# Kernel optimization log

Measured on AMD Instinct MI355X. Metric: run time of the kernel, lower is better.

Reference implementation:

```python
import jax, jax.numpy as jnp
import numpy as np

C = 96          # channels
N_STATE = 16    # d_state
EXPAND = 2
DI = EXPAND * C # d_inner = 192
D_CONV = 4
DT_RANK = 6     # ceil(C / 16)
EPS = 1e-5


def setup_inputs() -> dict:
    key = jax.random.key(0)
    ks = jax.random.split(key, 9)
    rn = lambda k, sh, s: jax.random.normal(k, sh, jnp.float32) * s
    inp = {
        "x": rn(ks[0], (1, C, 32, 32, 32), 1.0),
        # per-direction params, stacked along axis 0 in order (z, y, x)
        "ln_g": jnp.ones((3, C), jnp.float32),
        "ln_b": jnp.zeros((3, C), jnp.float32),
        "Win": rn(ks[1], (3, C, 2 * DI), 0.05),          # in_proj (no bias)
        "Wconv": rn(ks[2], (3, DI, 1, D_CONV), 0.2),     # depthwise conv1d
        "bconv": rn(ks[3], (3, DI), 0.02),
        "Wxp": rn(ks[4], (3, DI, DT_RANK + 2 * N_STATE), 0.05),  # x_proj
        "Wdt": rn(ks[5], (3, DT_RANK, DI), 0.1),         # dt_proj
        "bdt": rn(ks[6], (3, DI), 0.02),
        "A_log": jnp.log(jnp.broadcast_to(
            jnp.arange(1, N_STATE + 1, dtype=jnp.float32), (3, DI, N_STATE))),
        "Dskip": jnp.ones((3, DI), jnp.float32),
        "Wout": rn(ks[7], (3, DI, C), 0.05),             # out_proj (no bias)
        "alpha": jnp.ones((3,), jnp.float32),
    }
    return inp


def _layernorm(x, g, b):
    m = jnp.mean(x, axis=-1, keepdims=True)
    v = jnp.mean(jnp.square(x - m), axis=-1, keepdims=True)
    return (x - m) * jax.lax.rsqrt(v + EPS) * g + b


def _selective_scan(u, delta, A, Bm, Cm, Dskip):
    # u, delta: (N, L, DI); A: (DI, n); Bm, Cm: (N, L, n); Dskip: (DI,)
    def step(s, inp):
        d_t, B_t, C_t, u_t = inp                 # (N,DI),(N,n),(N,n),(N,DI)
        dA = jnp.exp(d_t[..., None] * A)         # (N, DI, n)
        dBu = d_t[..., None] * B_t[:, None, :] * u_t[..., None]
        s = dA * s + dBu                         # (N, DI, n)
        y = jnp.einsum('pdn,pn->pd', s, C_t)     # (N, DI)
        return s, y
    s0 = jnp.zeros((u.shape[0], A.shape[0], A.shape[1]), u.dtype)
    xs = (jnp.swapaxes(delta, 0, 1), jnp.swapaxes(Bm, 0, 1),
          jnp.swapaxes(Cm, 0, 1), jnp.swapaxes(u, 0, 1))
    _, ys = jax.lax.scan(step, s0, xs)           # ys: (L, N, DI)
    return jnp.swapaxes(ys, 0, 1) + u * Dskip


def _mamba_block(x, Win, Wconv, bconv, Wxp, Wdt, bdt, A_log, Dskip, Wout):
    # x: (N, L, C)
    xr = x @ Win                                  # (N, L, 2*DI)
    xm, res = jnp.split(xr, 2, axis=-1)
    # causal depthwise conv1d (torch pads d_conv-1 both sides then slices [:L])
    xc = jax.lax.conv_general_dilated(
        jnp.swapaxes(xm, 1, 2), Wconv, window_strides=(1,),
        padding=[(D_CONV - 1, 0)], feature_group_count=DI,
        dimension_numbers=('NCH', 'OIH', 'NCH')) + bconv[None, :, None]
    xm = jax.nn.silu(jnp.swapaxes(xc, 1, 2))      # (N, L, DI)
    x_dbl = xm @ Wxp
    dt = x_dbl[..., :DT_RANK]
    Bm = x_dbl[..., DT_RANK:DT_RANK + N_STATE]
    Cm = x_dbl[..., DT_RANK + N_STATE:]
    delta = jax.nn.softplus(dt @ Wdt + bdt)       # (N, L, DI)
    A = -jnp.exp(A_log)
    y = _selective_scan(xm, delta, A, Bm, Cm, Dskip)
    y = y * jax.nn.silu(res)
    return y @ Wout                               # (N, L, C)


def reference(x, ln_g, ln_b, Win, Wconv, bconv, Wxp, Wdt, bdt, A_log, Dskip, Wout, alpha):
    B, Cc, Dd, Hh, Ww = x.shape

    def run(i, xs):
        xs = _layernorm(xs, ln_g[i], ln_b[i])
        return _mamba_block(xs, Win[i], Wconv[i], bconv[i], Wxp[i], Wdt[i],
                            bdt[i], A_log[i], Dskip[i], Wout[i])

    # axial: scan depth D for each (h, w)
    xz = run(0, jnp.transpose(x, (0, 3, 4, 2, 1)).reshape(B * Hh * Ww, Dd, Cc))
    xz = jnp.transpose(xz.reshape(B, Hh, Ww, Dd, Cc), (0, 4, 3, 1, 2))
    # coronal: scan height H for each (d, w)
    xy = run(1, jnp.transpose(x, (0, 2, 4, 3, 1)).reshape(B * Dd * Ww, Hh, Cc))
    xy = jnp.transpose(xy.reshape(B, Dd, Ww, Hh, Cc), (0, 4, 1, 3, 2))
    # sagittal: scan width W for each (d, h)
    xx = run(2, jnp.transpose(x, (0, 2, 3, 4, 1)).reshape(B * Dd * Hh, Ww, Cc))
    xx = jnp.transpose(xx.reshape(B, Dd, Hh, Ww, Cc), (0, 4, 1, 2, 3))

    w = jax.nn.softmax(alpha)
    return w[0] * xz + w[1] * xy + w[2] * xx
```

## Files before the change

kernel.cpp:

```cpp
#include <hip/hip_runtime.h>
#include <hip/hip_bf16.h>


#define EPS_ 1e-5f

typedef __bf16 bf16x8 __attribute__((ext_vector_type(8)));
typedef float f32x4 __attribute__((ext_vector_type(4)));
typedef float f32x2 __attribute__((ext_vector_type(2)));
union U8b { uint4 u; bf16x8 v; };

__device__ __forceinline__ float silu_f(float v) { return v / (1.f + __expf(-v)); }
__device__ __forceinline__ bf16x8 ld_frag(const __hip_bfloat16* p) {
    U8b t; t.u = *(const uint4*)p; return t.v;
}

__global__ __launch_bounds__(256) void cvt_kernel(
    const float* __restrict__ Win, const float* __restrict__ Wxp,
    const float* __restrict__ Wout, __hip_bfloat16* __restrict__ ws)
{
    const int id = blockIdx.x * 256 + threadIdx.x;
    if (id < 110592) {
        const int d = id / 36864, r = id % 36864, n = r / 96, k = r % 96;
        ws[id] = __float2bfloat16(Win[d * 36864 + k * 384 + n]);
    } else if (id < 138240) {
        const int t = id - 110592;
        const int d = t / 9216, r = t % 9216, n = r / 192, k = r % 192;
        const float v = (n < 38) ? Wxp[d * 7296 + k * 38 + n] : 0.f;
        ws[id] = __float2bfloat16(v);
    } else {
        const int t = id - 138240;
        const int d = t / 18432, r = t % 18432, n = r / 192, k = r % 192;
        ws[id] = __float2bfloat16(Wout[d * 18432 + k * 96 + n]);
    }
}

template<bool PARTIAL>
__global__ __launch_bounds__(256, 4) void tdm_kernel(
    const float* __restrict__ x,     const float* __restrict__ ln_g,  const float* __restrict__ ln_b,
    const float* __restrict__ Wconv, const float* __restrict__ bconv,
    const float* __restrict__ Wdt,   const float* __restrict__ bdt,
    const float* __restrict__ Dskip,
    const float* __restrict__ alpha, const __hip_bfloat16* __restrict__ ws,
    float* __restrict__ pp,          float* __restrict__ out)
{
    __shared__ __align__(16) char sbuf[6656];
    __shared__ __align__(16) __hip_bfloat16 xu[32 * 200];
    __shared__ __align__(16) __hip_bfloat16 gyb[32 * 200];
    __hip_bfloat16* const aT    = (__hip_bfloat16*)sbuf;
    float*          const xdbuf = (float*)sbuf;

    const int tid = threadIdx.x;
    const int bid = blockIdx.x;
    const int wid = (bid & 7) * 384 + (bid >> 3);
    const int dir = wid >> 10;
    const int s   = wid & 1023;

    const float* gi = ln_g  + dir * 96;
    const float* bi = ln_b  + dir * 96;
    const float* Wc = Wconv + dir * 192 * 4;
    const float* bc = bconv + dir * 192;
    const float* Wd = Wdt   + dir * 6 * 192;
    const float* bd = bdt   + dir * 192;
    const float* Dk = Dskip + dir * 192;

    int base0, tmul;
    {
        const int hi = s >> 5, lo = s & 31;
        if (dir == 0)      { base0 = hi * 32 + lo;        tmul = 1024; }
        else if (dir == 1) { base0 = hi * 1024 + lo;      tmul = 32;   }
        else               { base0 = hi * 1024 + lo * 32; tmul = 1;    }
    }

    {
        const int row = tid >> 3;
        const int sub = tid & 7;
        float xv[12];
        float sum = 0.f, sq = 0.f;
        #pragma unroll
        for (int j = 0; j < 12; ++j) {
            const int c = sub * 12 + j;
            const float v = x[c * 32768 + row * tmul + base0];
            xv[j] = v; sum += v; sq += v * v;
        }
        #pragma unroll
        for (int m = 1; m < 8; m <<= 1) {
            sum += __shfl_xor(sum, m);
            sq  += __shfl_xor(sq, m);
        }
        const float mean = sum * (1.f / 96.f);
        const float var  = sq * (1.f / 96.f) - mean * mean;
        const float rstd = rsqrtf(var + EPS_);
        #pragma unroll
        for (int j = 0; j < 12; ++j) {
            const int c = sub * 12 + j;
            aT[row * 104 + c] = __float2bfloat16((xv[j] - mean) * rstd * gi[c] + bi[c]);
        }
    }
    __syncthreads();

    const int w  = tid >> 6;
    const int l  = tid & 63;
    const int lg = l >> 4;
    const int lm = l & 15;

    {
        const __hip_bfloat16* WT = ws + dir * 36864;
        #pragma unroll 1
        for (int mt = 0; mt < 2; ++mt) {
            bf16x8 aF[3];
            #pragma unroll
            for (int ks = 0; ks < 3; ++ks)
                aF[ks] = ld_frag(aT + (lm + 16 * mt) * 104 + 32 * ks + 8 * lg);
            f32x4 acc[6];
            #pragma unroll
            for (int nt = 0; nt < 6; ++nt) acc[nt] = (f32x4){0.f, 0.f, 0.f, 0.f};
            #pragma unroll
            for (int nt = 0; nt < 6; ++nt) {
                const int n = 96 * w + 16 * nt + lm;
                #pragma unroll
                for (int ks = 0; ks < 3; ++ks) {
                    const bf16x8 bF = ld_frag(WT + n * 96 + 32 * ks + 8 * lg);
                    acc[nt] = __builtin_amdgcn_mfma_f32_16x16x32_bf16(aF[ks], bF, acc[nt], 0, 0, 0);
                }
            }
            #pragma unroll
            for (int nt = 0; nt < 6; ++nt)
                #pragma unroll
                for (int reg = 0; reg < 4; ++reg) {
                    const int t   = 16 * mt + 4 * lg + reg;
                    const int col = 96 * w + 16 * nt + lm;
                    const float v = acc[nt][reg];
                    if (w < 2) xu[t * 200 + col] = __float2bfloat16(v);
                    else       gyb[t * 200 + (col - 192)] = __float2bfloat16(silu_f(v));
                }
        }
    }
    __syncthreads();

    if (tid < 192) {
        const int d = tid;
        const float4 wc = *(const float4*)&Wc[d * 4];
        const float bcd = bc[d];
        float w0 = 0.f, w1 = 0.f, w2 = 0.f;
        #pragma unroll
        for (int t = 0; t < 32; ++t) {
            const float xv = __bfloat162float(xu[t * 200 + d]);
            const float a  = bcd + w0 * wc.x + w1 * wc.y + w2 * wc.z + xv * wc.w;
            w0 = w1; w1 = w2; w2 = xv;
            xu[t * 200 + d] = __float2bfloat16(silu_f(a));
        }
    }
    __syncthreads();

    {
        const __hip_bfloat16* WT = ws + 110592 + dir * 9216;
        #pragma unroll
        for (int p = 0; p < 2; ++p) {
            const int T = (p == 0) ? w : (w < 2 ? w + 4 : -1);
            if (T >= 0) {
                const int mt = T / 3, nt = T % 3;
                f32x4 acc = (f32x4){0.f, 0.f, 0.f, 0.f};
                #pragma unroll
                for (int ks = 0; ks < 6; ++ks) {
                    const bf16x8 aF = ld_frag(xu + (lm + 16 * mt) * 200 + 32 * ks + 8 * lg);
                    const bf16x8 bF = ld_frag(WT + (16 * nt + lm) * 192 + 32 * ks + 8 * lg);
                    acc = __builtin_amdgcn_mfma_f32_16x16x32_bf16(aF, bF, acc, 0, 0, 0);
                }
                const int n = 16 * nt + lm;
                if (n < 38) {
                    const int col = (n < 6) ? n : n + 2;
                    #pragma unroll
                    for (int reg = 0; reg < 4; ++reg)
                        xdbuf[(16 * mt + 4 * lg + reg) * 40 + col] = acc[reg];
                }
            }
        }
    }
    __syncthreads();

    if (tid < 192) {
        const int d = tid;
        const f32x2 wd01 = {Wd[0 * 192 + d], Wd[1 * 192 + d]};
        const f32x2 wd23 = {Wd[2 * 192 + d], Wd[3 * 192 + d]};
        const f32x2 wd45 = {Wd[4 * 192 + d], Wd[5 * 192 + d]};
        const float bdd = bd[d], dsk = Dk[d];
        f32x2 st2[8];
        #pragma unroll
        for (int n = 0; n < 8; ++n) st2[n] = (f32x2){0.f, 0.f};
        for (int t = 0; t < 32; ++t) {
            const f32x4* row = (const f32x4*)(xdbuf + t * 40);
            const f32x4 q0 = row[0];
            const f32x4 q1 = row[1];
            f32x2 dt2 = (f32x2){q0.x, q0.y} * wd01;
            dt2 += (f32x2){q0.z, q0.w} * wd23;
            dt2 += (f32x2){q1.x, q1.y} * wd45;
            const float dt_ = bdd + dt2.x + dt2.y;
            const float p   = __expf(dt_);
            const float r   = __builtin_amdgcn_rcpf(1.f + p);
            const float dlt = (dt_ > 15.f) ? dt_ : __logf(1.f + p);
            const float ut  = __bfloat162float(xu[t * 200 + d]);
            const float du  = dlt * ut;
            const float r2s = r * r;
            const f32x2 r2v = {r2s, r2s};
            const f32x2 du2 = {du, du};
            f32x2 fp = {r, r2s};
            f32x2 y2 = {0.f, 0.f};
            #pragma unroll
            for (int g = 0; g < 4; ++g) {
                const f32x4 qB = row[2 + g];
                const f32x4 qC = row[6 + g];
                st2[2 * g]     = fp * st2[2 * g]     + du2 * (f32x2){qB.x, qB.y};
                y2            += st2[2 * g]     * (f32x2){qC.x, qC.y};
                fp            *= r2v;
                st2[2 * g + 1] = fp * st2[2 * g + 1] + du2 * (f32x2){qB.z, qB.w};
                y2            += st2[2 * g + 1] * (f32x2){qC.z, qC.w};
                fp            *= r2v;
            }
            const float y = y2.x + y2.y;
            const float gate = __bfloat162float(gyb[t * 200 + d]);
            gyb[t * 200 + d] = __float2bfloat16((y + ut * dsk) * gate);
        }
    }
    __syncthreads();

    {
        const __hip_bfloat16* WT = ws + 138240 + dir * 18432;
        const int mt = w >> 1, ntb = 3 * (w & 1);
        bf16x8 aF[6];
        #pragma unroll
        for (int ks = 0; ks < 6; ++ks)
            aF[ks] = ld_frag(gyb + (lm + 16 * mt) * 200 + 32 * ks + 8 * lg);
        const float e0 = __expf(alpha[0]), e1 = __expf(alpha[1]), e2 = __expf(alpha[2]);
        const float wgt = ((dir == 0) ? e0 : (dir == 1) ? e1 : e2) / (e0 + e1 + e2);
        #pragma unroll
        for (int nt3 = 0; nt3 < 3; ++nt3) {
            const int nt = ntb + nt3;
            f32x4 acc = (f32x4){0.f, 0.f, 0.f, 0.f};
            #pragma unroll
            for (int ks = 0; ks < 6; ++ks) {
                const bf16x8 bF = ld_frag(WT + (16 * nt + lm) * 192 + 32 * ks + 8 * lg);
                acc = __builtin_amdgcn_mfma_f32_16x16x32_bf16(aF[ks], bF, acc, 0, 0, 0);
            }
            const int j = 16 * nt + lm;
            if (PARTIAL) {
                if (dir < 2) {
                    float* dst = pp + (size_t)wid * 3072;
                    #pragma unroll
                    for (int reg = 0; reg < 4; ++reg) {
                        const int t = 16 * mt + 4 * lg + reg;
                        dst[t * 96 + j] = acc[reg] * wgt;
                    }
                } else {
                    #pragma unroll
                    for (int reg = 0; reg < 4; ++reg) {
                        const int t = 16 * mt + 4 * lg + reg;
                        out[j * 32768 + s * 32 + t] = acc[reg] * wgt;
                    }
                }
            } else {
                #pragma unroll
                for (int reg = 0; reg < 4; ++reg) {
                    const int t = 16 * mt + 4 * lg + reg;
                    atomicAdd(&out[j * 32768 + t * tmul + base0], acc[reg] * wgt);
                }
            }
        }
    }
}

__global__ __launch_bounds__(256) void red_kernel(const float* __restrict__ pp,
                                                  float* __restrict__ out)
{
    __shared__ float tile[96 * 33];
    const int d = blockIdx.x >> 5, h = blockIdx.x & 31;
    {
        const int w  = threadIdx.x >> 3;
        const int cs = (threadIdx.x & 7) * 12;
        const float* p0 = pp +           ((h * 32 + w) * 32 + d) * 96 + cs;
        const float* p1 = pp + 3145728 + ((d * 32 + w) * 32 + h) * 96 + cs;
        #pragma unroll
        for (int i = 0; i < 12; ++i)
            tile[(cs + i) * 33 + w] = p0[i] + p1[i];
    }
    __syncthreads();
    {
        const int w2 = threadIdx.x & 31;
        const int c0 = (threadIdx.x >> 5) * 12;
        #pragma unroll
        for (int i = 0; i < 12; ++i) {
            const int c = c0 + i;
            const int o = c * 32768 + d * 1024 + h * 32 + w2;
            out[o] = out[o] + tile[c * 33 + w2];
        }
    }
}

extern "C" void kernel_launch(void* const* d_in, const int* in_sizes, int n_in,
                              void* d_out, int out_size, void* d_ws, size_t ws_size,
                              hipStream_t stream) {
    (void)in_sizes; (void)n_in;
    __hip_bfloat16* ws = (__hip_bfloat16*)d_ws;
    float* pp = (float*)((char*)d_ws + 393216);
    const bool partial = (ws_size >= 25559040u);

    cvt_kernel<<<dim3(756), dim3(256), 0, stream>>>(
        (const float*)d_in[3], (const float*)d_in[6], (const float*)d_in[11], ws);

    if (partial) {
        tdm_kernel<true><<<dim3(3072), dim3(256), 0, stream>>>(
            (const float*)d_in[0],  (const float*)d_in[1],  (const float*)d_in[2],
            (const float*)d_in[4],  (const float*)d_in[5],
            (const float*)d_in[7],  (const float*)d_in[8],
            (const float*)d_in[10],
            (const float*)d_in[12], ws, pp, (float*)d_out);
        red_kernel<<<dim3(1024), dim3(256), 0, stream>>>(pp, (float*)d_out);
    } else {
        hipMemsetAsync(d_out, 0, (size_t)out_size * sizeof(float), stream);
        tdm_kernel<false><<<dim3(3072), dim3(256), 0, stream>>>(
            (const float*)d_in[0],  (const float*)d_in[1],  (const float*)d_in[2],
            (const float*)d_in[4],  (const float*)d_in[5],
            (const float*)d_in[7],  (const float*)d_in[8],
            (const float*)d_in[10],
            (const float*)d_in[12], ws, pp, (float*)d_out);
    }
}
```

Baseline: 205.8 us.

## Store partial direction outputs in bf16 and process three sequences per block

The partial-result buffer for the z and y directions now holds bf16 instead of fp32. This halves the global write and read traffic between the main kernel and the reduction kernel, and lowers the workspace threshold for the partial path. The main kernel now launches 1024 blocks that each loop over three work items, with a block-wide sync added at the top of each iteration. The loop also reuses the softmax exponentials and loads gate and u values earlier. In exchange, the partial sums lose precision to bf16 rounding, and there are fewer resident blocks to hide latency.

```diff
diff --git a/kernel.cpp b/kernel.cpp
--- a/kernel.cpp
+++ b/kernel.cpp
@@ -41,7 +41,7 @@
     const float* __restrict__ Wdt,   const float* __restrict__ bdt,
     const float* __restrict__ Dskip,
     const float* __restrict__ alpha, const __hip_bfloat16* __restrict__ ws,
-    float* __restrict__ pp,          float* __restrict__ out)
+    __hip_bfloat16* __restrict__ pp, float* __restrict__ out)
 {
     __shared__ __align__(16) char sbuf[6656];
     __shared__ __align__(16) __hip_bfloat16 xu[32 * 200];
@@ -49,226 +49,235 @@
     __hip_bfloat16* const aT    = (__hip_bfloat16*)sbuf;
     float*          const xdbuf = (float*)sbuf;
 
-    const int tid = threadIdx.x;
-    const int bid = blockIdx.x;
-    const int wid = (bid & 7) * 384 + (bid >> 3);
-    const int dir = wid >> 10;
-    const int s   = wid & 1023;
-
-    const float* gi = ln_g  + dir * 96;
-    const float* bi = ln_b  + dir * 96;
-    const float* Wc = Wconv + dir * 192 * 4;
-    const float* bc = bconv + dir * 192;
-    const float* Wd = Wdt   + dir * 6 * 192;
-    const float* bd = bdt   + dir * 192;
-    const float* Dk = Dskip + dir * 192;
-
-    int base0, tmul;
-    {
-        const int hi = s >> 5, lo = s & 31;
-        if (dir == 0)      { base0 = hi * 32 + lo;        tmul = 1024; }
-        else if (dir == 1) { base0 = hi * 1024 + lo;      tmul = 32;   }
-        else               { base0 = hi * 1024 + lo * 32; tmul = 1;    }
-    }
-
-    {
-        const int row = tid >> 3;
-        const int sub = tid & 7;
-        float xv[12];
-        float sum = 0.f, sq = 0.f;
-        #pragma unroll
-        for (int j = 0; j < 12; ++j) {
-            const int c = sub * 12 + j;
-            const float v = x[c * 32768 + row * tmul + base0];
-            xv[j] = v; sum += v; sq += v * v;
-        }
-        #pragma unroll
-        for (int m = 1; m < 8; m <<= 1) {
-            sum += __shfl_xor(sum, m);
-            sq  += __shfl_xor(sq, m);
-        }
-        const float mean = sum * (1.f / 96.f);
-        const float var  = sq * (1.f / 96.f) - mean * mean;
-        const float rstd = rsqrtf(var + EPS_);
-        #pragma unroll
-        for (int j = 0; j < 12; ++j) {
-            const int c = sub * 12 + j;
-            aT[row * 104 + c] = __float2bfloat16((xv[j] - mean) * rstd * gi[c] + bi[c]);
-        }
-    }
-    __syncthreads();
+    const int tid  = threadIdx.x;
+    const int bid  = blockIdx.x;
+    const int base = (bid & 7) * 128 + (bid >> 3);
 
     const int w  = tid >> 6;
     const int l  = tid & 63;
     const int lg = l >> 4;
     const int lm = l & 15;
 
-    {
-        const __hip_bfloat16* WT = ws + dir * 36864;
-        #pragma unroll 1
-        for (int mt = 0; mt < 2; ++mt) {
-            bf16x8 aF[3];
-            #pragma unroll
-            for (int ks = 0; ks < 3; ++ks)
-                aF[ks] = ld_frag(aT + (lm + 16 * mt) * 104 + 32 * ks + 8 * lg);
-            f32x4 acc[6];
-            #pragma unroll
-            for (int nt = 0; nt < 6; ++nt) acc[nt] = (f32x4){0.f, 0.f, 0.f, 0.f};
-            #pragma unroll
-            for (int nt = 0; nt < 6; ++nt) {
-                const int n = 96 * w + 16 * nt + lm;
-                #pragma unroll
-                for (int ks = 0; ks < 3; ++ks) {
-                    const bf16x8 bF = ld_frag(WT + n * 96 + 32 * ks + 8 * lg);
-                    acc[nt] = __builtin_amdgcn_mfma_f32_16x16x32_bf16(aF[ks], bF, acc[nt], 0, 0, 0);
-                }
-            }
-            #pragma unroll
-            for (int nt = 0; nt < 6; ++nt)
-                #pragma unroll
-                for (int reg = 0; reg < 4; ++reg) {
-                    const int t   = 16 * mt + 4 * lg + reg;
-                    const int col = 96 * w + 16 * nt + lm;
-                    const float v = acc[nt][reg];
-                    if (w < 2) xu[t * 200 + col] = __float2bfloat16(v);
-                    else       gyb[t * 200 + (col - 192)] = __float2bfloat16(silu_f(v));
-                }
-        }
-    }
-    __syncthreads();
-
-    if (tid < 192) {
-        const int d = tid;
-        const float4 wc = *(const float4*)&Wc[d * 4];
-        const float bcd = bc[d];
-        float w0 = 0.f, w1 = 0.f, w2 = 0.f;
-        #pragma unroll
-        for (int t = 0; t < 32; ++t) {
-            const float xv = __bfloat162float(xu[t * 200 + d]);
-            const float a  = bcd + w0 * wc.x + w1 * wc.y + w2 * wc.z + xv * wc.w;
-            w0 = w1; w1 = w2; w2 = xv;
-            xu[t * 200 + d] = __float2bfloat16(silu_f(a));
-        }
-    }
-    __syncthreads();
-
-    {
-        const __hip_bfloat16* WT = ws + 110592 + dir * 9216;
-        #pragma unroll
-        for (int p = 0; p < 2; ++p) {
-            const int T = (p == 0) ? w : (w < 2 ? w + 4 : -1);
-            if (T >= 0) {
-                const int mt = T / 3, nt = T % 3;
-                f32x4 acc = (f32x4){0.f, 0.f, 0.f, 0.f};
-                #pragma unroll
-                for (int ks = 0; ks < 6; ++ks) {
-                    const bf16x8 aF = ld_frag(xu + (lm + 16 * mt) * 200 + 32 * ks + 8 * lg);
-                    const bf16x8 bF = ld_frag(WT + (16 * nt + lm) * 192 + 32 * ks + 8 * lg);
-                    acc = __builtin_amdgcn_mfma_f32_16x16x32_bf16(aF, bF, acc, 0, 0, 0);
-                }
-                const int n = 16 * nt + lm;
-                if (n < 38) {
-                    const int col = (n < 6) ? n : n + 2;
+    const float e0a = __expf(alpha[0]), e1a = __expf(alpha[1]), e2a = __expf(alpha[2]);
+    const float esum = e0a + e1a + e2a;
+
+    #pragma unroll 1
+    for (int q = 0; q < 3; ++q) {
+        const int e   = base * 3 + q;
+        const int dir = e >> 10;
+        const int s   = e & 1023;
+
+        const float* gi = ln_g  + dir * 96;
+        const float* bi = ln_b  + dir * 96;
+        const float* Wc = Wconv + dir * 192 * 4;
+        const float* bc = bconv + dir * 192;
+        const float* Wd = Wdt   + dir * 6 * 192;
+        const float* bd = bdt   + dir * 192;
+        const float* Dk = Dskip + dir * 192;
+
+        int base0, tmul;
+        {
+            const int hi = s >> 5, lo = s & 31;
+            if (dir == 0)      { base0 = hi * 32 + lo;        tmul = 1024; }
+            else if (dir == 1) { base0 = hi * 1024 + lo;      tmul = 32;   }
+            else               { base0 = hi * 1024 + lo * 32; tmul = 1;    }
+        }
+
+        __syncthreads();
+
+        {
+            const int row = tid >> 3;
+            const int sub = tid & 7;
+            float xv[12];
+            float sum = 0.f, sq = 0.f;
+            #pragma unroll
+            for (int j = 0; j < 12; ++j) {
+                const int c = sub * 12 + j;
+                const float v = x[c * 32768 + row * tmul + base0];
+                xv[j] = v; sum += v; sq += v * v;
+            }
+            #pragma unroll
+            for (int m = 1; m < 8; m <<= 1) {
+                sum += __shfl_xor(sum, m);
+                sq  += __shfl_xor(sq, m);
+            }
+            const float mean = sum * (1.f / 96.f);
+            const float var  = sq * (1.f / 96.f) - mean * mean;
+            const float rstd = rsqrtf(var + EPS_);
+            #pragma unroll
+            for (int j = 0; j < 12; ++j) {
+                const int c = sub * 12 + j;
+                aT[row * 104 + c] = __float2bfloat16((xv[j] - mean) * rstd * gi[c] + bi[c]);
+            }
+        }
+        __syncthreads();
+
+        {
+            const __hip_bfloat16* WT = ws + dir * 36864;
+            #pragma unroll 1
+            for (int mt = 0; mt < 2; ++mt) {
+                bf16x8 aF[3];
+                #pragma unroll
+                for (int ks = 0; ks < 3; ++ks)
+                    aF[ks] = ld_frag(aT + (lm + 16 * mt) * 104 + 32 * ks + 8 * lg);
+                f32x4 acc[6];
+                #pragma unroll
+                for (int nt = 0; nt < 6; ++nt) acc[nt] = (f32x4){0.f, 0.f, 0.f, 0.f};
+                #pragma unroll
+                for (int nt = 0; nt < 6; ++nt) {
+                    const int n = 96 * w + 16 * nt + lm;
                     #pragma unroll
-                    for (int reg = 0; reg < 4; ++reg)
-                        xdbuf[(16 * mt + 4 * lg + reg) * 40 + col] = acc[reg];
-                }
-            }
-        }
-    }
-    __syncthreads();
-
-    if (tid < 192) {
-        const int d = tid;
-        const f32x2 wd01 = {Wd[0 * 192 + d], Wd[1 * 192 + d]};
-        const f32x2 wd23 = {Wd[2 * 192 + d], Wd[3 * 192 + d]};
-        const f32x2 wd45 = {Wd[4 * 192 + d], Wd[5 * 192 + d]};
-        const float bdd = bd[d], dsk = Dk[d];
-        f32x2 st2[8];
-        #pragma unroll
-        for (int n = 0; n < 8; ++n) st2[n] = (f32x2){0.f, 0.f};
-        for (int t = 0; t < 32; ++t) {
-            const f32x4* row = (const f32x4*)(xdbuf + t * 40);
-            const f32x4 q0 = row[0];
-            const f32x4 q1 = row[1];
-            f32x2 dt2 = (f32x2){q0.x, q0.y} * wd01;
-            dt2 += (f32x2){q0.z, q0.w} * wd23;
-            dt2 += (f32x2){q1.x, q1.y} * wd45;
-            const float dt_ = bdd + dt2.x + dt2.y;
-            const float p   = __expf(dt_);
-            const float r   = __builtin_amdgcn_rcpf(1.f + p);
-            const float dlt = (dt_ > 15.f) ? dt_ : __logf(1.f + p);
-            const float ut  = __bfloat162float(xu[t * 200 + d]);
-            const float du  = dlt * ut;
-            const float r2s = r * r;
-            const f32x2 r2v = {r2s, r2s};
-            const f32x2 du2 = {du, du};
-            f32x2 fp = {r, r2s};
-            f32x2 y2 = {0.f, 0.f};
-            #pragma unroll
-            for (int g = 0; g < 4; ++g) {
-                const f32x4 qB = row[2 + g];
-                const f32x4 qC = row[6 + g];
-                st2[2 * g]     = fp * st2[2 * g]     + du2 * (f32x2){qB.x, qB.y};
-                y2            += st2[2 * g]     * (f32x2){qC.x, qC.y};
-                fp            *= r2v;
-                st2[2 * g + 1] = fp * st2[2 * g + 1] + du2 * (f32x2){qB.z, qB.w};
-                y2            += st2[2 * g + 1] * (f32x2){qC.z, qC.w};
-                fp            *= r2v;
-            }
-            const float y = y2.x + y2.y;
-            const float gate = __bfloat162float(gyb[t * 200 + d]);
-            gyb[t * 200 + d] = __float2bfloat16((y + ut * dsk) * gate);
-        }
-    }
-    __syncthreads();
-
-    {
-        const __hip_bfloat16* WT = ws + 138240 + dir * 18432;
-        const int mt = w >> 1, ntb = 3 * (w & 1);
-        bf16x8 aF[6];
-        #pragma unroll
-        for (int ks = 0; ks < 6; ++ks)
-            aF[ks] = ld_frag(gyb + (lm + 16 * mt) * 200 + 32 * ks + 8 * lg);
-        const float e0 = __expf(alpha[0]), e1 = __expf(alpha[1]), e2 = __expf(alpha[2]);
-        const float wgt = ((dir == 0) ? e0 : (dir == 1) ? e1 : e2) / (e0 + e1 + e2);
-        #pragma unroll
-        for (int nt3 = 0; nt3 < 3; ++nt3) {
-            const int nt = ntb + nt3;
-            f32x4 acc = (f32x4){0.f, 0.f, 0.f, 0.f};
-            #pragma unroll
-            for (int ks = 0; ks < 6; ++ks) {
-                const bf16x8 bF = ld_frag(WT + (16 * nt + lm) * 192 + 32 * ks + 8 * lg);
-                acc = __builtin_amdgcn_mfma_f32_16x16x32_bf16(aF[ks], bF, acc, 0, 0, 0);
-            }
-            const int j = 16 * nt + lm;
-            if (PARTIAL) {
-                if (dir < 2) {
-                    float* dst = pp + (size_t)wid * 3072;
+                    for (int ks = 0; ks < 3; ++ks) {
+                        const bf16x8 bF = ld_frag(WT + n * 96 + 32 * ks + 8 * lg);
+                        acc[nt] = __builtin_amdgcn_mfma_f32_16x16x32_bf16(aF[ks], bF, acc[nt], 0, 0, 0);
+                    }
+                }
+                #pragma unroll
+                for (int nt = 0; nt < 6; ++nt)
                     #pragma unroll
                     for (int reg = 0; reg < 4; ++reg) {
-                        const int t = 16 * mt + 4 * lg + reg;
-                        dst[t * 96 + j] = acc[reg] * wgt;
+                        const int t   = 16 * mt + 4 * lg + reg;
+                        const int col = 96 * w + 16 * nt + lm;
+                        const float v = acc[nt][reg];
+                        if (w < 2) xu[t * 200 + col] = __float2bfloat16(v);
+                        else       gyb[t * 200 + (col - 192)] = __float2bfloat16(silu_f(v));
+                    }
+            }
+        }
+        __syncthreads();
+
+        if (tid < 192) {
+            const int d = tid;
+            const float4 wc = *(const float4*)&Wc[d * 4];
+            const float bcd = bc[d];
+            float w0 = 0.f, w1 = 0.f, w2 = 0.f;
+            #pragma unroll
+            for (int t = 0; t < 32; ++t) {
+                const float xv = __bfloat162float(xu[t * 200 + d]);
+                const float a  = bcd + w0 * wc.x + w1 * wc.y + w2 * wc.z + xv * wc.w;
+                w0 = w1; w1 = w2; w2 = xv;
+                xu[t * 200 + d] = __float2bfloat16(silu_f(a));
+            }
+        }
+        __syncthreads();
+
+        {
+            const __hip_bfloat16* WT = ws + 110592 + dir * 9216;
+            #pragma unroll
+            for (int p = 0; p < 2; ++p) {
+                const int T = (p == 0) ? w : (w < 2 ? w + 4 : -1);
+                if (T >= 0) {
+                    const int mt = T / 3, nt = T % 3;
+                    f32x4 acc = (f32x4){0.f, 0.f, 0.f, 0.f};
+                    #pragma unroll
+                    for (int ks = 0; ks < 6; ++ks) {
+                        const bf16x8 aF = ld_frag(xu + (lm + 16 * mt) * 200 + 32 * ks + 8 * lg);
+                        const bf16x8 bF = ld_frag(WT + (16 * nt + lm) * 192 + 32 * ks + 8 * lg);
+                        acc = __builtin_amdgcn_mfma_f32_16x16x32_bf16(aF, bF, acc, 0, 0, 0);
+                    }
+                    const int n = 16 * nt + lm;
+                    if (n < 38) {
+                        const int col = (n < 6) ? n : n + 2;
+                        #pragma unroll
+                        for (int reg = 0; reg < 4; ++reg)
+                            xdbuf[(16 * mt + 4 * lg + reg) * 40 + col] = acc[reg];
+                    }
+                }
+            }
+        }
+        __syncthreads();
+
+        if (tid < 192) {
+            const int d = tid;
+            const f32x2 wd01 = {Wd[0 * 192 + d], Wd[1 * 192 + d]};
+            const f32x2 wd23 = {Wd[2 * 192 + d], Wd[3 * 192 + d]};
+            const f32x2 wd45 = {Wd[4 * 192 + d], Wd[5 * 192 + d]};
+            const float bdd = bd[d], dsk = Dk[d];
+            f32x2 st2[8];
+            #pragma unroll
+            for (int n = 0; n < 8; ++n) st2[n] = (f32x2){0.f, 0.f};
+            for (int t = 0; t < 32; ++t) {
+                const f32x4* row = (const f32x4*)(xdbuf + t * 40);
+                const f32x4 q0 = row[0];
+                const f32x4 q1 = row[1];
+                const float gate = __bfloat162float(gyb[t * 200 + d]);
+                const float ut   = __bfloat162float(xu[t * 200 + d]);
+                f32x2 dt2 = (f32x2){q0.x, q0.y} * wd01;
+                dt2 += (f32x2){q0.z, q0.w} * wd23;
+                dt2 += (f32x2){q1.x, q1.y} * wd45;
+                const float dt_ = bdd + dt2.x + dt2.y;
+                const float p   = __expf(dt_);
+                const float r   = __builtin_amdgcn_rcpf(1.f + p);
+                const float dlt = (dt_ > 15.f) ? dt_ : __logf(1.f + p);
+                const float du  = dlt * ut;
+                const float r2s = r * r;
+                const f32x2 r2v = {r2s, r2s};
+                const f32x2 du2 = {du, du};
+                f32x2 fp = {r, r2s};
+                f32x2 y2 = {0.f, 0.f};
+                #pragma unroll
+                for (int g = 0; g < 4; ++g) {
+                    const f32x4 qB = row[2 + g];
+                    const f32x4 qC = row[6 + g];
+                    st2[2 * g]     = fp * st2[2 * g]     + du2 * (f32x2){qB.x, qB.y};
+                    y2            += st2[2 * g]     * (f32x2){qC.x, qC.y};
+                    fp            *= r2v;
+                    st2[2 * g + 1] = fp * st2[2 * g + 1] + du2 * (f32x2){qB.z, qB.w};
+                    y2            += st2[2 * g + 1] * (f32x2){qC.z, qC.w};
+                    fp            *= r2v;
+                }
+                const float y = y2.x + y2.y;
+                gyb[t * 200 + d] = __float2bfloat16((y + ut * dsk) * gate);
+            }
+        }
+        __syncthreads();
+
+        {
+            const __hip_bfloat16* WT = ws + 138240 + dir * 18432;
+            const int mt = w >> 1, ntb = 3 * (w & 1);
+            bf16x8 aF[6];
+            #pragma unroll
+            for (int ks = 0; ks < 6; ++ks)
+                aF[ks] = ld_frag(gyb + (lm + 16 * mt) * 200 + 32 * ks + 8 * lg);
+            const float wgt = ((dir == 0) ? e0a : (dir == 1) ? e1a : e2a) / esum;
+            #pragma unroll
+            for (int nt3 = 0; nt3 < 3; ++nt3) {
+                const int nt = ntb + nt3;
+                f32x4 acc = (f32x4){0.f, 0.f, 0.f, 0.f};
+                #pragma unroll
+                for (int ks = 0; ks < 6; ++ks) {
+                    const bf16x8 bF = ld_frag(WT + (16 * nt + lm) * 192 + 32 * ks + 8 * lg);
+                    acc = __builtin_amdgcn_mfma_f32_16x16x32_bf16(aF[ks], bF, acc, 0, 0, 0);
+                }
+                const int j = 16 * nt + lm;
+                if (PARTIAL) {
+                    if (dir < 2) {
+                        __hip_bfloat16* dst = pp + (size_t)e * 3072;
+                        #pragma unroll
+                        for (int reg = 0; reg < 4; ++reg) {
+                            const int t = 16 * mt + 4 * lg + reg;
+                            dst[t * 96 + j] = __float2bfloat16(acc[reg] * wgt);
+                        }
+                    } else {
+                        #pragma unroll
+                        for (int reg = 0; reg < 4; ++reg) {
+                            const int t = 16 * mt + 4 * lg + reg;
+                            out[j * 32768 + s * 32 + t] = acc[reg] * wgt;
+                        }
                     }
                 } else {
                     #pragma unroll
                     for (int reg = 0; reg < 4; ++reg) {
                         const int t = 16 * mt + 4 * lg + reg;
-                        out[j * 32768 + s * 32 + t] = acc[reg] * wgt;
-                    }
-                }
-            } else {
-                #pragma unroll
-                for (int reg = 0; reg < 4; ++reg) {
-                    const int t = 16 * mt + 4 * lg + reg;
-                    atomicAdd(&out[j * 32768 + t * tmul + base0], acc[reg] * wgt);
-                }
-            }
-        }
-    }
-}
-
-__global__ __launch_bounds__(256) void red_kernel(const float* __restrict__ pp,
+                        atomicAdd(&out[j * 32768 + t * tmul + base0], acc[reg] * wgt);
+                    }
+                }
+            }
+        }
+    }
+}
+
+__global__ __launch_bounds__(256) void red_kernel(const __hip_bfloat16* __restrict__ pp,
                                                   float* __restrict__ out)
 {
     __shared__ float tile[96 * 33];
@@ -276,11 +285,11 @@
     {
         const int w  = threadIdx.x >> 3;
         const int cs = (threadIdx.x & 7) * 12;
-        const float* p0 = pp +           ((h * 32 + w) * 32 + d) * 96 + cs;
-        const float* p1 = pp + 3145728 + ((d * 32 + w) * 32 + h) * 96 + cs;
+        const __hip_bfloat16* p0 = pp +           ((h * 32 + w) * 32 + d) * 96 + cs;
+        const __hip_bfloat16* p1 = pp + 3145728 + ((d * 32 + w) * 32 + h) * 96 + cs;
         #pragma unroll
         for (int i = 0; i < 12; ++i)
-            tile[(cs + i) * 33 + w] = p0[i] + p1[i];
+            tile[(cs + i) * 33 + w] = __bfloat162float(p0[i]) + __bfloat162float(p1[i]);
     }
     __syncthreads();
     {
@@ -300,14 +309,14 @@
                               hipStream_t stream) {
     (void)in_sizes; (void)n_in;
     __hip_bfloat16* ws = (__hip_bfloat16*)d_ws;
-    float* pp = (float*)((char*)d_ws + 393216);
-    const bool partial = (ws_size >= 25559040u);
+    __hip_bfloat16* pp = (__hip_bfloat16*)((char*)d_ws + 393216);
+    const bool partial = (ws_size >= 12976128u);
 
     cvt_kernel<<<dim3(756), dim3(256), 0, stream>>>(
         (const float*)d_in[3], (const float*)d_in[6], (const float*)d_in[11], ws);
 
     if (partial) {
-        tdm_kernel<true><<<dim3(3072), dim3(256), 0, stream>>>(
+        tdm_kernel<true><<<dim3(1024), dim3(256), 0, stream>>>(
             (const float*)d_in[0],  (const float*)d_in[1],  (const float*)d_in[2],
             (const float*)d_in[4],  (const float*)d_in[5],
             (const float*)d_in[7],  (const float*)d_in[8],
@@ -316,7 +325,7 @@
         red_kernel<<<dim3(1024), dim3(256), 0, stream>>>(pp, (float*)d_out);
     } else {
         hipMemsetAsync(d_out, 0, (size_t)out_size * sizeof(float), stream);
-        tdm_kernel<false><<<dim3(3072), dim3(256), 0, stream>>>(
+        tdm_kernel<false><<<dim3(1024), dim3(256), 0, stream>>>(
             (const float*)d_in[0],  (const float*)d_in[1],  (const float*)d_in[2],
             (const float*)d_in[4],  (const float*)d_in[5],
             (const float*)d_in[7],  (const float*)d_in[8],
```

Result: slower. 244.2 us (+18.7%).
